# Kernel optimization log

Measured on AMD Instinct MI355X. Metric: run time of the kernel, lower is better.

## Reference

```python
import jax, jax.numpy as jnp
import numpy as np

TOPK = 8
NMS_K = 5
SIGMA = 3.0


def _mlp2(x, w1, b1, w2, b2):
    return jnp.maximum(x @ w1 + b1, 0.0) @ w2 + b2


def _l2norm(x):
    n = jnp.linalg.norm(x, axis=-1, keepdims=True)
    return x / jnp.maximum(n, 1e-12)


def _bilinear_sample(fm, ys, xs):
    # fm: (V, C, Hf, Wf); ys, xs: (V, K) float sample positions (align_corners=True,
    # zero padding outside [0, size-1], matching F.grid_sample defaults).
    V, C, Hf, Wf = fm.shape
    y0f = jnp.floor(ys)
    x0f = jnp.floor(xs)
    wy = ys - y0f  # (V, K)
    wx = xs - x0f
    y0 = y0f.astype(jnp.int32)
    x0 = x0f.astype(jnp.int32)

    def gather(yi, xi):
        valid = ((yi >= 0) & (yi < Hf) & (xi >= 0) & (xi < Wf)).astype(fm.dtype)  # (V,K)
        yc = jnp.clip(yi, 0, Hf - 1)
        xc = jnp.clip(xi, 0, Wf - 1)
        v = jax.vmap(lambda f, y, x: f[:, y, x])(fm, yc, xc)  # (V, C, K)
        return v * valid[:, None, :]

    out = (gather(y0, x0) * ((1 - wy) * (1 - wx))[:, None, :]
           + gather(y0, x0 + 1) * ((1 - wy) * wx)[:, None, :]
           + gather(y0 + 1, x0) * (wy * (1 - wx))[:, None, :]
           + gather(y0 + 1, x0 + 1) * (wy * wx)[:, None, :])
    return out.transpose(0, 2, 1)  # (V, K, C)


def _forward(heatmap, feature_map, prev_node_embed,
             n1_w, n1_b, n2_w, n2_b, p1_w, p1_b, p2_w, p2_b,
             c_w, c_b, s_w, s_b):
    bs, nc, _, H, W = heatmap.shape
    hm = heatmap.reshape(bs * nc, H, W)

    # ---- PeakExtractor: maxpool NMS + topk ----
    pad = NMS_K // 2
    pooled = jax.lax.reduce_window(hm, -jnp.inf, jax.lax.max,
                                   (1, NMS_K, NMS_K), (1, 1, 1),
                                   ((0, 0), (pad, pad), (pad, pad)))
    hm_nms = hm * (hm == pooled).astype(hm.dtype)
    vals, idxs = jax.lax.top_k(hm_nms.reshape(bs * nc, H * W), TOPK)
    rows = idxs // W
    cols = idxs % W
    peak_coords = jnp.stack([rows, cols], axis=-1).reshape(bs, nc, TOPK, 2)

    # ---- NodeEmbeddingHead: grid_sample gather + MLP ----
    V, C, Hf, Wf = feature_map.shape
    ys = rows[:V].astype(jnp.float32) * (Hf / H)
    xs = cols[:V].astype(jnp.float32) * (Wf / W)
    sampled = _bilinear_sample(feature_map, ys, xs)  # (V, K, C)
    peak_node_embeds = _l2norm(_mlp2(sampled, n1_w, n1_b, n2_w, n2_b))  # (V, K, D)

    # ---- pooled node embed ----
    pooled_feat = feature_map.mean(axis=(0, 2, 3))  # (C,)
    curr_node_embed = _l2norm(_mlp2(pooled_feat[None, :], p1_w, p1_b, p2_w, p2_b))  # (1, D)

    # ---- TransitionScorer ----
    D = prev_node_embed.shape[-1]
    prev_e = jnp.broadcast_to(prev_node_embed, (V, D))
    curr_e = jnp.broadcast_to(curr_node_embed, (V, D))
    context = jnp.maximum(jnp.concatenate([prev_e, curr_e], axis=-1) @ c_w + c_b, 0.0)
    proto = context @ s_w + s_b  # (V, D)
    transition_scores = jnp.einsum('vkd,vd->vk', peak_node_embeds, proto)  # (V, K)
    peak_weights = jax.nn.softmax(transition_scores, axis=-1)

    # ---- separable gaussian bias (vectorized over views and peaks) ----
    coords0 = peak_coords[0, :V].astype(jnp.float32)  # (V, K, 2)
    rr = jnp.arange(H, dtype=jnp.float32)
    cc = jnp.arange(W, dtype=jnp.float32)
    inv2s2 = 1.0 / (2.0 * SIGMA ** 2)
    gr = jnp.exp(-((rr[None, None, :] - coords0[..., 0:1]) ** 2) * inv2s2)  # (V,K,H)
    gc = jnp.exp(-((cc[None, None, :] - coords0[..., 1:2]) ** 2) * inv2s2)  # (V,K,W)
    bias = jnp.einsum('vkh,vkw,vk->vhw', gr, gc, peak_weights)  # (V,H,W)
    reweighted = heatmap + bias[None, :, None]  # (bs, nc, 1, H, W)

    return reweighted, curr_node_embed, peak_coords, transition_scores, peak_node_embeds


def setup_inputs() -> dict:
    key = jax.random.key(0)
    ks = jax.random.split(key, 16)
    C, D = 128, 64
    inp = {
        'heatmap': jax.random.normal(ks[0], (1, 16, 1, 1024, 1024), jnp.float32),
        'feature_map': jax.random.normal(ks[1], (16, 128, 32, 32), jnp.float32),
        'prev_node_embed': jax.random.normal(ks[2], (1, D), jnp.float32),
        'n1_w': jax.random.normal(ks[3], (C, D), jnp.float32) * 0.05,
        'n1_b': jax.random.normal(ks[4], (D,), jnp.float32) * 0.05,
        'n2_w': jax.random.normal(ks[5], (D, D), jnp.float32) * 0.05,
        'n2_b': jax.random.normal(ks[6], (D,), jnp.float32) * 0.05,
        'p1_w': jax.random.normal(ks[7], (C, D), jnp.float32) * 0.05,
        'p1_b': jax.random.normal(ks[8], (D,), jnp.float32) * 0.05,
        'p2_w': jax.random.normal(ks[9], (D, D), jnp.float32) * 0.05,
        'p2_b': jax.random.normal(ks[10], (D,), jnp.float32) * 0.05,
        'c_w': jax.random.normal(ks[11], (2 * D, D), jnp.float32) * 0.05,
        'c_b': jax.random.normal(ks[12], (D,), jnp.float32) * 0.05,
        's_w': jax.random.normal(ks[13], (D, D), jnp.float32) * 0.05,
        's_b': jax.random.normal(ks[14], (D,), jnp.float32) * 0.05,
    }
    return inp


def reference(heatmap, feature_map, prev_node_embed,
              n1_w, n1_b, n2_w, n2_b, p1_w, p1_b, p2_w, p2_b,
              c_w, c_b, s_w, s_b):
    return _forward(heatmap, feature_map, prev_node_embed,
                    n1_w, n1_b, n2_w, n2_b, p1_w, p1_b, p2_w, p2_b,
                    c_w, c_b, s_w, s_b)
```

## Files before the change

### kernel.cpp

```cpp
#include <hip/hip_runtime.h>
#include <math.h>

#define HH 1024
#define WW 1024
#define NCH 16
#define ROWS_PER_BLOCK 8
#define BLOCKS_PER_CH (HH / ROWS_PER_BLOCK)
#define NEG_INF (-INFINITY)

__device__ __forceinline__ bool better_f(float v1, int i1, float v2, int i2) {
    return (v1 > v2) || ((v1 == v2) && (i1 < i2));
}

__global__ __launch_bounds__(256) void kA(const float* __restrict__ hm,
                                          float* __restrict__ out,
                                          float* __restrict__ cand_val,
                                          int* __restrict__ cand_idx) {
    const int ch = blockIdx.y;
    const int r0 = blockIdx.x * ROWS_PER_BLOCK;
    const int tid = threadIdx.x;
    const int c0 = tid * 4;
    const float* hmc = hm + (size_t)ch * (size_t)(HH * WW);
    float* outc = out + (size_t)ch * (size_t)(HH * WW);

    float4 rawv[5], hxv[5];
    float tv[8]; int ti[8];
#pragma unroll
    for (int j = 0; j < 8; ++j) { tv[j] = NEG_INF; ti[j] = 0x7FFFFFFF; }

    auto loadrow = [&](int r, float4& rv, float4& hv) {
        if (r < 0 || r >= HH) {
            rv = make_float4(NEG_INF, NEG_INF, NEG_INF, NEG_INF);
            hv = rv;
            return;
        }
        const float* rp = hmc + (size_t)r * WW;
        float4 M = *(const float4*)(rp + c0);
        float4 L = (c0 >= 4) ? *(const float4*)(rp + c0 - 4)
                             : make_float4(NEG_INF, NEG_INF, NEG_INF, NEG_INF);
        float4 R = (c0 + 4 < WW) ? *(const float4*)(rp + c0 + 4)
                                 : make_float4(NEG_INF, NEG_INF, NEG_INF, NEG_INF);
        float v2 = L.z, v3 = L.w, v4 = M.x, v5 = M.y, v6 = M.z, v7 = M.w, v8 = R.x, v9 = R.y;
        float a = fmaxf(v2, v3), b = fmaxf(v4, v5), c = fmaxf(v6, v7), d = fmaxf(v8, v9);
        hv.x = fmaxf(fmaxf(a, b), v6);
        hv.y = fmaxf(fmaxf(v3, b), c);
        hv.z = fmaxf(fmaxf(b, c), v8);
        hv.w = fmaxf(fmaxf(v5, c), d);
        rv = M;
    };

    auto push = [&](float v, int ix) {
        if (better_f(v, ix, tv[7], ti[7])) {
            tv[7] = v; ti[7] = ix;
#pragma unroll
            for (int j = 7; j >= 1; --j) {
                if (better_f(tv[j], ti[j], tv[j - 1], ti[j - 1])) {
                    float fv = tv[j]; tv[j] = tv[j - 1]; tv[j - 1] = fv;
                    int iv = ti[j]; ti[j] = ti[j - 1]; ti[j - 1] = iv;
                }
            }
        }
    };

    loadrow(r0 - 2, rawv[0], hxv[0]);
    loadrow(r0 - 1, rawv[1], hxv[1]);
    loadrow(r0 + 0, rawv[2], hxv[2]);
    loadrow(r0 + 1, rawv[3], hxv[3]);

#pragma unroll
    for (int i = 0; i < ROWS_PER_BLOCK; ++i) {
        const int r = r0 + i;
        loadrow(r + 2, rawv[(4 + i) % 5], hxv[(4 + i) % 5]);
        float4 p;
        p.x = fmaxf(fmaxf(fmaxf(hxv[0].x, hxv[1].x), fmaxf(hxv[2].x, hxv[3].x)), hxv[4].x);
        p.y = fmaxf(fmaxf(fmaxf(hxv[0].y, hxv[1].y), fmaxf(hxv[2].y, hxv[3].y)), hxv[4].y);
        p.z = fmaxf(fmaxf(fmaxf(hxv[0].z, hxv[1].z), fmaxf(hxv[2].z, hxv[3].z)), hxv[4].z);
        p.w = fmaxf(fmaxf(fmaxf(hxv[0].w, hxv[1].w), fmaxf(hxv[2].w, hxv[3].w)), hxv[4].w);
        float4 cen = rawv[(2 + i) % 5];
        *(float4*)(outc + (size_t)r * WW + c0) = cen;
        int base = r * WW + c0;
        push((cen.x == p.x) ? cen.x : 0.0f, base + 0);
        push((cen.y == p.y) ? cen.y : 0.0f, base + 1);
        push((cen.z == p.z) ? cen.z : 0.0f, base + 2);
        push((cen.w == p.w) ? cen.w : 0.0f, base + 3);
    }

    __shared__ float swv[2][4];
    __shared__ int swi[2][4];
    const int lane = tid & 63, wid = tid >> 6;
    float wv = 0.f; int wi = 0;
    for (int rnd = 0; rnd < 8; ++rnd) {
        float v = tv[0]; int ix = ti[0];
#pragma unroll
        for (int off = 32; off >= 1; off >>= 1) {
            float ov = __shfl_xor(v, off);
            int oi = __shfl_xor(ix, off);
            if (better_f(ov, oi, v, ix)) { v = ov; ix = oi; }
        }
        if (lane == 0) { swv[rnd & 1][wid] = v; swi[rnd & 1][wid] = ix; }
        __syncthreads();
        float bv = swv[rnd & 1][0]; int bi = swi[rnd & 1][0];
        if (better_f(swv[rnd & 1][1], swi[rnd & 1][1], bv, bi)) { bv = swv[rnd & 1][1]; bi = swi[rnd & 1][1]; }
        if (better_f(swv[rnd & 1][2], swi[rnd & 1][2], bv, bi)) { bv = swv[rnd & 1][2]; bi = swi[rnd & 1][2]; }
        if (better_f(swv[rnd & 1][3], swi[rnd & 1][3], bv, bi)) { bv = swv[rnd & 1][3]; bi = swi[rnd & 1][3]; }
        if (ti[0] == bi) {
#pragma unroll
            for (int j = 0; j < 7; ++j) { tv[j] = tv[j + 1]; ti[j] = ti[j + 1]; }
            tv[7] = NEG_INF; ti[7] = 0x7FFFFFFF;
        }
        if (tid == rnd) { wv = bv; wi = bi; }
    }
    const int slotbase = (ch * BLOCKS_PER_CH + blockIdx.x) * 8;
    if (tid < 8) { cand_val[slotbase + tid] = wv; cand_idx[slotbase + tid] = wi; }
}

__global__ __launch_bounds__(64) void kB(const float* __restrict__ cand_val,
                                         const int* __restrict__ cand_idx,
                                         float* __restrict__ out_pc,
                                         int* __restrict__ ws_rows,
                                         int* __restrict__ ws_cols) {
    const int ch = blockIdx.x;
    const int lane = threadIdx.x;
    float tv[8]; int ti[8];
#pragma unroll
    for (int j = 0; j < 8; ++j) { tv[j] = NEG_INF; ti[j] = 0x7FFFFFFF; }
    auto push = [&](float v, int ix) {
        if (better_f(v, ix, tv[7], ti[7])) {
            tv[7] = v; ti[7] = ix;
#pragma unroll
            for (int j = 7; j >= 1; --j) {
                if (better_f(tv[j], ti[j], tv[j - 1], ti[j - 1])) {
                    float fv = tv[j]; tv[j] = tv[j - 1]; tv[j - 1] = fv;
                    int iv = ti[j]; ti[j] = ti[j - 1]; ti[j - 1] = iv;
                }
            }
        }
    };
    const float* cv = cand_val + (size_t)ch * 1024 + lane * 16;
    const int* ci = cand_idx + (size_t)ch * 1024 + lane * 16;
#pragma unroll
    for (int j = 0; j < 16; ++j) push(cv[j], ci[j]);

    int mywin = 0;
    for (int rnd = 0; rnd < 8; ++rnd) {
        float v = tv[0]; int ix = ti[0];
#pragma unroll
        for (int off = 32; off >= 1; off >>= 1) {
            float ov = __shfl_xor(v, off);
            int oi = __shfl_xor(ix, off);
            if (better_f(ov, oi, v, ix)) { v = ov; ix = oi; }
        }
        if (ti[0] == ix) {
#pragma unroll
            for (int j = 0; j < 7; ++j) { tv[j] = tv[j + 1]; ti[j] = ti[j + 1]; }
            tv[7] = NEG_INF; ti[7] = 0x7FFFFFFF;
        }
        if (lane == rnd) mywin = ix;
    }
    if (lane < 8) {
        int row = mywin >> 10;
        int col = mywin & 1023;
        out_pc[ch * 16 + lane * 2 + 0] = (float)row;
        out_pc[ch * 16 + lane * 2 + 1] = (float)col;
        ws_rows[ch * 8 + lane] = row;
        ws_cols[ch * 8 + lane] = col;
    }
}

__global__ __launch_bounds__(256) void kC(const float* __restrict__ fm,
                                          float* __restrict__ pooled) {
    const int c = blockIdx.x;
    const int tid = threadIdx.x;
    float s = 0.f;
    for (int v = 0; v < 16; ++v) {
        const float* p = fm + (size_t)v * 131072 + (size_t)c * 1024;
#pragma unroll
        for (int i = 0; i < 4; ++i) s += p[tid + i * 256];
    }
#pragma unroll
    for (int off = 32; off >= 1; off >>= 1) s += __shfl_xor(s, off);
    __shared__ float red[4];
    if ((tid & 63) == 0) red[tid >> 6] = s;
    __syncthreads();
    if (tid == 0) pooled[c] = (red[0] + red[1] + red[2] + red[3]) * (1.0f / 16384.0f);
}

__global__ __launch_bounds__(64) void kD0(const float* __restrict__ pooled,
                                          const float* __restrict__ prev,
                                          const float* __restrict__ p1w, const float* __restrict__ p1b,
                                          const float* __restrict__ p2w, const float* __restrict__ p2b,
                                          const float* __restrict__ cw, const float* __restrict__ cb,
                                          const float* __restrict__ sw, const float* __restrict__ sb,
                                          float* __restrict__ out_curr,
                                          float* __restrict__ ws_proto) {
    const int j = threadIdx.x;
    __shared__ float h1[64], cshr[64], ctx[64];
    float acc = p1b[j];
    for (int c = 0; c < 128; ++c) acc = fmaf(pooled[c], p1w[c * 64 + j], acc);
    h1[j] = fmaxf(acc, 0.f);
    __syncthreads();
    float e = p2b[j];
    for (int m = 0; m < 64; ++m) e = fmaf(h1[m], p2w[m * 64 + j], e);
    float sq = e * e;
#pragma unroll
    for (int off = 32; off >= 1; off >>= 1) sq += __shfl_xor(sq, off);
    float cur = e / fmaxf(sqrtf(sq), 1e-12f);
    out_curr[j] = cur;
    cshr[j] = cur;
    __syncthreads();
    float a3 = cb[j];
    for (int i = 0; i < 64; ++i) a3 = fmaf(prev[i], cw[i * 64 + j], a3);
    for (int i = 0; i < 64; ++i) a3 = fmaf(cshr[i], cw[(64 + i) * 64 + j], a3);
    ctx[j] = fmaxf(a3, 0.f);
    __syncthreads();
    float a4 = sb[j];
    for (int m = 0; m < 64; ++m) a4 = fmaf(ctx[m], sw[m * 64 + j], a4);
    ws_proto[j] = a4;
}

__global__ __launch_bounds__(64) void kD1(const float* __restrict__ fm,
                                          const int* __restrict__ ws_rows,
                                          const int* __restrict__ ws_cols,
                                          const float* __restrict__ n1w, const float* __restrict__ n1b,
                                          const float* __restrict__ n2w, const float* __restrict__ n2b,
                                          const float* __restrict__ ws_proto,
                                          float* __restrict__ out_ts,
                                          float* __restrict__ out_pe) {
    const int p = blockIdx.x;
    const int v = p >> 3, k = p & 7;
    const int j = threadIdx.x;
    __shared__ float s[128], h1[64];
    const float* base = fm + (size_t)v * 131072;

    int row = ws_rows[v * 8 + k], col = ws_cols[v * 8 + k];
    float ys = (float)row * 0.03125f, xs = (float)col * 0.03125f;
    int y0 = (int)floorf(ys), x0 = (int)floorf(xs);
    float wy = ys - (float)y0, wx = xs - (float)x0;
    float w00 = (1.f - wy) * (1.f - wx), w01 = (1.f - wy) * wx;
    float w10 = wy * (1.f - wx), w11 = wy * wx;

    auto samp = [&](int c) -> float {
        const float* fc = base + (size_t)c * 1024;
        float r = fc[y0 * 32 + x0] * w00;
        if (x0 + 1 < 32) r += fc[y0 * 32 + x0 + 1] * w01;
        if (y0 + 1 < 32) {
            r += fc[(y0 + 1) * 32 + x0] * w10;
            if (x0 + 1 < 32) r += fc[(y0 + 1) * 32 + x0 + 1] * w11;
        }
        return r;
    };
    s[j] = samp(j);
    s[j + 64] = samp(j + 64);
    __syncthreads();
    float a = n1b[j];
    for (int c = 0; c < 128; ++c) a = fmaf(s[c], n1w[c * 64 + j], a);
    h1[j] = fmaxf(a, 0.f);
    __syncthreads();
    float e = n2b[j];
    for (int m = 0; m < 64; ++m) e = fmaf(h1[m], n2w[m * 64 + j], e);
    float sq = e * e;
#pragma unroll
    for (int off = 32; off >= 1; off >>= 1) sq += __shfl_xor(sq, off);
    float emb = e / fmaxf(sqrtf(sq), 1e-12f);
    out_pe[(size_t)p * 64 + j] = emb;
    float sc = emb * ws_proto[j];
#pragma unroll
    for (int off = 32; off >= 1; off >>= 1) sc += __shfl_xor(sc, off);
    if (j == 0) out_ts[p] = sc;
}

__global__ __launch_bounds__(256) void kF(const int* __restrict__ ws_rows,
                                          const int* __restrict__ ws_cols,
                                          const float* __restrict__ ts,
                                          float* __restrict__ out) {
    const int p = blockIdx.x;
    const int v = p >> 3, k = p & 7;
    const int tid = threadIdx.x;
    float t[8];
#pragma unroll
    for (int i = 0; i < 8; ++i) t[i] = ts[v * 8 + i];
    float m = t[0];
#pragma unroll
    for (int i = 1; i < 8; ++i) m = fmaxf(m, t[i]);
    float sum = 0.f;
#pragma unroll
    for (int i = 0; i < 8; ++i) sum += __expf(t[i] - m);
    const float pw = __expf(t[k] - m) / sum;

    const int r = ws_rows[v * 8 + k], c = ws_cols[v * 8 + k];
    float* oc = out + (size_t)v * (size_t)(HH * WW);
    const float inv2s2 = 1.0f / 18.0f;
    const int RAD = 32, SZ = 65;
    for (int idx = tid; idx < SZ * SZ; idx += 256) {
        int dy = idx / SZ - RAD, dx = idx % SZ - RAD;
        int py = r + dy, px = c + dx;
        if (py >= 0 && py < HH && px >= 0 && px < WW) {
            float d2 = (float)(dy * dy + dx * dx);
            atomicAdd(&oc[(size_t)py * WW + px], pw * __expf(-d2 * inv2s2));
        }
    }
}

extern "C" void kernel_launch(void* const* d_in, const int* in_sizes, int n_in,
                              void* d_out, int out_size, void* d_ws, size_t ws_size,
                              hipStream_t stream) {
    (void)in_sizes; (void)n_in; (void)out_size; (void)ws_size;
    const float* hm   = (const float*)d_in[0];
    const float* fm   = (const float*)d_in[1];
    const float* prev = (const float*)d_in[2];
    const float* n1w  = (const float*)d_in[3];
    const float* n1b  = (const float*)d_in[4];
    const float* n2w  = (const float*)d_in[5];
    const float* n2b  = (const float*)d_in[6];
    const float* p1w  = (const float*)d_in[7];
    const float* p1b  = (const float*)d_in[8];
    const float* p2w  = (const float*)d_in[9];
    const float* p2b  = (const float*)d_in[10];
    const float* cw   = (const float*)d_in[11];
    const float* cb   = (const float*)d_in[12];
    const float* sw   = (const float*)d_in[13];
    const float* sb   = (const float*)d_in[14];
    float* out = (float*)d_out;

    char* ws = (char*)d_ws;
    float* cand_val  = (float*)(ws + 0);
    int*   cand_idx  = (int*)(ws + 65536);
    int*   ws_rows   = (int*)(ws + 131072);
    int*   ws_cols   = (int*)(ws + 131584);
    float* ws_pooled = (float*)(ws + 132096);
    float* ws_proto  = (float*)(ws + 132608);

    float* out_rew  = out;
    float* out_curr = out + 16777216;
    float* out_pc   = out + 16777280;
    float* out_ts   = out + 16777536;
    float* out_pe   = out + 16777664;

    kA<<<dim3(BLOCKS_PER_CH, NCH), 256, 0, stream>>>(hm, out_rew, cand_val, cand_idx);
    kB<<<NCH, 64, 0, stream>>>(cand_val, cand_idx, out_pc, ws_rows, ws_cols);
    kC<<<128, 256, 0, stream>>>(fm, ws_pooled);
    kD0<<<1, 64, 0, stream>>>(ws_pooled, prev, p1w, p1b, p2w, p2b, cw, cb, sw, sb,
                              out_curr, ws_proto);
    kD1<<<128, 64, 0, stream>>>(fm, ws_rows, ws_cols, n1w, n1b, n2w, n2b, ws_proto,
                                out_ts, out_pe);
    kF<<<128, 256, 0, stream>>>(ws_rows, ws_cols, out_ts, out_rew);
}
```

Baseline: 206.8 us.

## Fuse tail kernels, use lane shuffles for NMS halo, drop splat atomics

Combines the candidate merge with feature pooling, and the prototype MLP, node embedding and Gaussian splat into one block per view. This cuts six launches to three and lets the splat use plain read-modify-write under block barriers instead of atomics. kA now gets its horizontal halo from wavefront shuffles rather than two extra float4 loads, and the top-8 lists become named scalars so they stay in registers. The cost is that the prototype MLP is recomputed in each of the 16 blocks and the splat phase runs on only 16 blocks, which lowers parallelism there.

```diff
diff --git a/kernel.cpp b/kernel.cpp
--- a/kernel.cpp
+++ b/kernel.cpp
@@ -11,6 +11,52 @@
 __device__ __forceinline__ bool better_f(float v1, int i1, float v2, int i2) {
     return (v1 > v2) || ((v1 == v2) && (i1 < i2));
 }
+
+#define CSWAP(J, JM) \
+    if (better_f(tv##J, ti##J, tv##JM, ti##JM)) { \
+        float _fv = tv##J; tv##J = tv##JM; tv##JM = _fv; \
+        int _iv = ti##J; ti##J = ti##JM; ti##JM = _iv; }
+
+#define PUSH(VAL, IDX) do { \
+    float _pv = (VAL); int _pix = (IDX); \
+    if (better_f(_pv, _pix, tv7, ti7)) { \
+        tv7 = _pv; ti7 = _pix; \
+        CSWAP(7,6) CSWAP(6,5) CSWAP(5,4) CSWAP(4,3) CSWAP(3,2) CSWAP(2,1) CSWAP(1,0) \
+    } } while (0)
+
+#define POP() do { \
+    tv0=tv1; ti0=ti1; tv1=tv2; ti1=ti2; tv2=tv3; ti2=ti3; tv3=tv4; ti3=ti4; \
+    tv4=tv5; ti4=ti5; tv5=tv6; ti5=ti6; tv6=tv7; ti6=ti7; \
+    tv7=NEG_INF; ti7=0x7FFFFFFF; } while (0)
+
+#define TOP8_INIT() \
+    float tv0=NEG_INF,tv1=NEG_INF,tv2=NEG_INF,tv3=NEG_INF,tv4=NEG_INF,tv5=NEG_INF,tv6=NEG_INF,tv7=NEG_INF; \
+    int ti0=0x7FFFFFFF,ti1=0x7FFFFFFF,ti2=0x7FFFFFFF,ti3=0x7FFFFFFF,ti4=0x7FFFFFFF,ti5=0x7FFFFFFF,ti6=0x7FFFFFFF,ti7=0x7FFFFFFF;
+
+#define LOADROW(R, RV, HV) do { \
+    const int _r = (R); \
+    if (_r < 0 || _r >= HH) { \
+        RV = make_float4(NEG_INF, NEG_INF, NEG_INF, NEG_INF); HV = RV; \
+    } else { \
+        const float* _rp = hmc + (size_t)_r * WW; \
+        float4 _M = *(const float4*)(_rp + c0); \
+        float _lm2 = __shfl_up(_M.z, 1), _lm1 = __shfl_up(_M.w, 1); \
+        float _rp0 = __shfl_down(_M.x, 1), _rp1 = __shfl_down(_M.y, 1); \
+        if (lane == 0) { \
+            _lm2 = (c0 >= 2) ? _rp[c0 - 2] : NEG_INF; \
+            _lm1 = (c0 >= 1) ? _rp[c0 - 1] : NEG_INF; \
+        } \
+        if (lane == 63) { \
+            _rp0 = (c0 + 4 < WW) ? _rp[c0 + 4] : NEG_INF; \
+            _rp1 = (c0 + 5 < WW) ? _rp[c0 + 5] : NEG_INF; \
+        } \
+        float _m01 = fmaxf(_M.x, _M.y), _m23 = fmaxf(_M.z, _M.w); \
+        HV.x = fmaxf(fmaxf(_lm2, _lm1), fmaxf(_m01, _M.z)); \
+        HV.y = fmaxf(_lm1, fmaxf(_m01, _m23)); \
+        HV.z = fmaxf(fmaxf(_m01, _m23), _rp0); \
+        HV.w = fmaxf(fmaxf(_M.y, _m23), fmaxf(_rp0, _rp1)); \
+        RV = _M; \
+    } } while (0)
 
 __global__ __launch_bounds__(256) void kA(const float* __restrict__ hm,
                                           float* __restrict__ out,
@@ -19,78 +65,46 @@
     const int ch = blockIdx.y;
     const int r0 = blockIdx.x * ROWS_PER_BLOCK;
     const int tid = threadIdx.x;
+    const int lane = tid & 63;
     const int c0 = tid * 4;
     const float* hmc = hm + (size_t)ch * (size_t)(HH * WW);
     float* outc = out + (size_t)ch * (size_t)(HH * WW);
 
-    float4 rawv[5], hxv[5];
-    float tv[8]; int ti[8];
-#pragma unroll
-    for (int j = 0; j < 8; ++j) { tv[j] = NEG_INF; ti[j] = 0x7FFFFFFF; }
-
-    auto loadrow = [&](int r, float4& rv, float4& hv) {
-        if (r < 0 || r >= HH) {
-            rv = make_float4(NEG_INF, NEG_INF, NEG_INF, NEG_INF);
-            hv = rv;
-            return;
-        }
-        const float* rp = hmc + (size_t)r * WW;
-        float4 M = *(const float4*)(rp + c0);
-        float4 L = (c0 >= 4) ? *(const float4*)(rp + c0 - 4)
-                             : make_float4(NEG_INF, NEG_INF, NEG_INF, NEG_INF);
-        float4 R = (c0 + 4 < WW) ? *(const float4*)(rp + c0 + 4)
-                                 : make_float4(NEG_INF, NEG_INF, NEG_INF, NEG_INF);
-        float v2 = L.z, v3 = L.w, v4 = M.x, v5 = M.y, v6 = M.z, v7 = M.w, v8 = R.x, v9 = R.y;
-        float a = fmaxf(v2, v3), b = fmaxf(v4, v5), c = fmaxf(v6, v7), d = fmaxf(v8, v9);
-        hv.x = fmaxf(fmaxf(a, b), v6);
-        hv.y = fmaxf(fmaxf(v3, b), c);
-        hv.z = fmaxf(fmaxf(b, c), v8);
-        hv.w = fmaxf(fmaxf(v5, c), d);
-        rv = M;
-    };
-
-    auto push = [&](float v, int ix) {
-        if (better_f(v, ix, tv[7], ti[7])) {
-            tv[7] = v; ti[7] = ix;
-#pragma unroll
-            for (int j = 7; j >= 1; --j) {
-                if (better_f(tv[j], ti[j], tv[j - 1], ti[j - 1])) {
-                    float fv = tv[j]; tv[j] = tv[j - 1]; tv[j - 1] = fv;
-                    int iv = ti[j]; ti[j] = ti[j - 1]; ti[j - 1] = iv;
-                }
-            }
-        }
-    };
-
-    loadrow(r0 - 2, rawv[0], hxv[0]);
-    loadrow(r0 - 1, rawv[1], hxv[1]);
-    loadrow(r0 + 0, rawv[2], hxv[2]);
-    loadrow(r0 + 1, rawv[3], hxv[3]);
+    TOP8_INIT();
+
+    float4 raw0, raw1, raw2, raw3, raw4;
+    float4 hx0, hx1, hx2, hx3, hx4;
+    LOADROW(r0 - 2, raw0, hx0);
+    LOADROW(r0 - 1, raw1, hx1);
+    LOADROW(r0 + 0, raw2, hx2);
+    LOADROW(r0 + 1, raw3, hx3);
 
 #pragma unroll
     for (int i = 0; i < ROWS_PER_BLOCK; ++i) {
         const int r = r0 + i;
-        loadrow(r + 2, rawv[(4 + i) % 5], hxv[(4 + i) % 5]);
+        LOADROW(r + 2, raw4, hx4);
         float4 p;
-        p.x = fmaxf(fmaxf(fmaxf(hxv[0].x, hxv[1].x), fmaxf(hxv[2].x, hxv[3].x)), hxv[4].x);
-        p.y = fmaxf(fmaxf(fmaxf(hxv[0].y, hxv[1].y), fmaxf(hxv[2].y, hxv[3].y)), hxv[4].y);
-        p.z = fmaxf(fmaxf(fmaxf(hxv[0].z, hxv[1].z), fmaxf(hxv[2].z, hxv[3].z)), hxv[4].z);
-        p.w = fmaxf(fmaxf(fmaxf(hxv[0].w, hxv[1].w), fmaxf(hxv[2].w, hxv[3].w)), hxv[4].w);
-        float4 cen = rawv[(2 + i) % 5];
+        p.x = fmaxf(fmaxf(fmaxf(hx0.x, hx1.x), fmaxf(hx2.x, hx3.x)), hx4.x);
+        p.y = fmaxf(fmaxf(fmaxf(hx0.y, hx1.y), fmaxf(hx2.y, hx3.y)), hx4.y);
+        p.z = fmaxf(fmaxf(fmaxf(hx0.z, hx1.z), fmaxf(hx2.z, hx3.z)), hx4.z);
+        p.w = fmaxf(fmaxf(fmaxf(hx0.w, hx1.w), fmaxf(hx2.w, hx3.w)), hx4.w);
+        float4 cen = raw2;
         *(float4*)(outc + (size_t)r * WW + c0) = cen;
         int base = r * WW + c0;
-        push((cen.x == p.x) ? cen.x : 0.0f, base + 0);
-        push((cen.y == p.y) ? cen.y : 0.0f, base + 1);
-        push((cen.z == p.z) ? cen.z : 0.0f, base + 2);
-        push((cen.w == p.w) ? cen.w : 0.0f, base + 3);
+        PUSH((cen.x == p.x) ? cen.x : 0.0f, base + 0);
+        PUSH((cen.y == p.y) ? cen.y : 0.0f, base + 1);
+        PUSH((cen.z == p.z) ? cen.z : 0.0f, base + 2);
+        PUSH((cen.w == p.w) ? cen.w : 0.0f, base + 3);
+        raw0 = raw1; raw1 = raw2; raw2 = raw3; raw3 = raw4;
+        hx0 = hx1; hx1 = hx2; hx2 = hx3; hx3 = hx4;
     }
 
     __shared__ float swv[2][4];
     __shared__ int swi[2][4];
-    const int lane = tid & 63, wid = tid >> 6;
+    const int wid = tid >> 6;
     float wv = 0.f; int wi = 0;
     for (int rnd = 0; rnd < 8; ++rnd) {
-        float v = tv[0]; int ix = ti[0];
+        float v = tv0; int ix = ti0;
 #pragma unroll
         for (int off = 32; off >= 1; off >>= 1) {
             float ov = __shfl_xor(v, off);
@@ -103,109 +117,101 @@
         if (better_f(swv[rnd & 1][1], swi[rnd & 1][1], bv, bi)) { bv = swv[rnd & 1][1]; bi = swi[rnd & 1][1]; }
         if (better_f(swv[rnd & 1][2], swi[rnd & 1][2], bv, bi)) { bv = swv[rnd & 1][2]; bi = swi[rnd & 1][2]; }
         if (better_f(swv[rnd & 1][3], swi[rnd & 1][3], bv, bi)) { bv = swv[rnd & 1][3]; bi = swi[rnd & 1][3]; }
-        if (ti[0] == bi) {
-#pragma unroll
-            for (int j = 0; j < 7; ++j) { tv[j] = tv[j + 1]; ti[j] = ti[j + 1]; }
-            tv[7] = NEG_INF; ti[7] = 0x7FFFFFFF;
-        }
+        if (ti0 == bi) POP();
         if (tid == rnd) { wv = bv; wi = bi; }
     }
     const int slotbase = (ch * BLOCKS_PER_CH + blockIdx.x) * 8;
     if (tid < 8) { cand_val[slotbase + tid] = wv; cand_idx[slotbase + tid] = wi; }
 }
 
-__global__ __launch_bounds__(64) void kB(const float* __restrict__ cand_val,
-                                         const int* __restrict__ cand_idx,
-                                         float* __restrict__ out_pc,
-                                         int* __restrict__ ws_rows,
-                                         int* __restrict__ ws_cols) {
-    const int ch = blockIdx.x;
-    const int lane = threadIdx.x;
-    float tv[8]; int ti[8];
-#pragma unroll
-    for (int j = 0; j < 8; ++j) { tv[j] = NEG_INF; ti[j] = 0x7FFFFFFF; }
-    auto push = [&](float v, int ix) {
-        if (better_f(v, ix, tv[7], ti[7])) {
-            tv[7] = v; ti[7] = ix;
-#pragma unroll
-            for (int j = 7; j >= 1; --j) {
-                if (better_f(tv[j], ti[j], tv[j - 1], ti[j - 1])) {
-                    float fv = tv[j]; tv[j] = tv[j - 1]; tv[j - 1] = fv;
-                    int iv = ti[j]; ti[j] = ti[j - 1]; ti[j - 1] = iv;
-                }
+__global__ __launch_bounds__(256) void kBC(const float* __restrict__ cand_val,
+                                           const int* __restrict__ cand_idx,
+                                           const float* __restrict__ fm,
+                                           float* __restrict__ out_pc,
+                                           int* __restrict__ ws_rows,
+                                           int* __restrict__ ws_cols,
+                                           float* __restrict__ pooled) {
+    const int tid = threadIdx.x;
+    if (blockIdx.x < 16) {
+        if (tid >= 64) return;
+        const int ch = blockIdx.x;
+        const int lane = tid;
+        TOP8_INIT();
+        const float* cv = cand_val + (size_t)ch * 1024 + lane * 16;
+        const int* ci = cand_idx + (size_t)ch * 1024 + lane * 16;
+#pragma unroll
+        for (int j = 0; j < 16; ++j) PUSH(cv[j], ci[j]);
+
+        int mywin = 0;
+        for (int rnd = 0; rnd < 8; ++rnd) {
+            float v = tv0; int ix = ti0;
+#pragma unroll
+            for (int off = 32; off >= 1; off >>= 1) {
+                float ov = __shfl_xor(v, off);
+                int oi = __shfl_xor(ix, off);
+                if (better_f(ov, oi, v, ix)) { v = ov; ix = oi; }
             }
-        }
-    };
-    const float* cv = cand_val + (size_t)ch * 1024 + lane * 16;
-    const int* ci = cand_idx + (size_t)ch * 1024 + lane * 16;
-#pragma unroll
-    for (int j = 0; j < 16; ++j) push(cv[j], ci[j]);
-
-    int mywin = 0;
-    for (int rnd = 0; rnd < 8; ++rnd) {
-        float v = tv[0]; int ix = ti[0];
-#pragma unroll
-        for (int off = 32; off >= 1; off >>= 1) {
-            float ov = __shfl_xor(v, off);
-            int oi = __shfl_xor(ix, off);
-            if (better_f(ov, oi, v, ix)) { v = ov; ix = oi; }
-        }
-        if (ti[0] == ix) {
-#pragma unroll
-            for (int j = 0; j < 7; ++j) { tv[j] = tv[j + 1]; ti[j] = ti[j + 1]; }
-            tv[7] = NEG_INF; ti[7] = 0x7FFFFFFF;
-        }
-        if (lane == rnd) mywin = ix;
-    }
-    if (lane < 8) {
-        int row = mywin >> 10;
-        int col = mywin & 1023;
-        out_pc[ch * 16 + lane * 2 + 0] = (float)row;
-        out_pc[ch * 16 + lane * 2 + 1] = (float)col;
-        ws_rows[ch * 8 + lane] = row;
-        ws_cols[ch * 8 + lane] = col;
-    }
-}
-
-__global__ __launch_bounds__(256) void kC(const float* __restrict__ fm,
-                                          float* __restrict__ pooled) {
-    const int c = blockIdx.x;
+            if (ti0 == ix) POP();
+            if (lane == rnd) mywin = ix;
+        }
+        if (lane < 8) {
+            int row = mywin >> 10;
+            int col = mywin & 1023;
+            out_pc[ch * 16 + lane * 2 + 0] = (float)row;
+            out_pc[ch * 16 + lane * 2 + 1] = (float)col;
+            ws_rows[ch * 8 + lane] = row;
+            ws_cols[ch * 8 + lane] = col;
+        }
+    } else {
+        const int c = blockIdx.x - 16;
+        float s = 0.f;
+        for (int v = 0; v < 16; ++v) {
+            const float* p = fm + (size_t)v * 131072 + (size_t)c * 1024;
+#pragma unroll
+            for (int i = 0; i < 4; ++i) s += p[tid + i * 256];
+        }
+#pragma unroll
+        for (int off = 32; off >= 1; off >>= 1) s += __shfl_xor(s, off);
+        __shared__ float red[4];
+        if ((tid & 63) == 0) red[tid >> 6] = s;
+        __syncthreads();
+        if (tid == 0) pooled[c] = (red[0] + red[1] + red[2] + red[3]) * (1.0f / 16384.0f);
+    }
+}
+
+__global__ __launch_bounds__(256) void kDF(const float* __restrict__ fm,
+                                           const int* __restrict__ ws_rows,
+                                           const int* __restrict__ ws_cols,
+                                           const float* __restrict__ n1w, const float* __restrict__ n1b,
+                                           const float* __restrict__ n2w, const float* __restrict__ n2b,
+                                           const float* __restrict__ p1w, const float* __restrict__ p1b,
+                                           const float* __restrict__ p2w, const float* __restrict__ p2b,
+                                           const float* __restrict__ cw, const float* __restrict__ cb,
+                                           const float* __restrict__ sw, const float* __restrict__ sb,
+                                           const float* __restrict__ prev,
+                                           const float* __restrict__ pooled,
+                                           float* __restrict__ out_curr,
+                                           float* __restrict__ out_ts,
+                                           float* __restrict__ out_pe,
+                                           float* __restrict__ out_rew) {
+    const int v = blockIdx.x;
     const int tid = threadIdx.x;
-    float s = 0.f;
-    for (int v = 0; v < 16; ++v) {
-        const float* p = fm + (size_t)v * 131072 + (size_t)c * 1024;
-#pragma unroll
-        for (int i = 0; i < 4; ++i) s += p[tid + i * 256];
-    }
-#pragma unroll
-    for (int off = 32; off >= 1; off >>= 1) s += __shfl_xor(s, off);
-    __shared__ float red[4];
-    if ((tid & 63) == 0) red[tid >> 6] = s;
-    __syncthreads();
-    if (tid == 0) pooled[c] = (red[0] + red[1] + red[2] + red[3]) * (1.0f / 16384.0f);
-}
-
-__global__ __launch_bounds__(64) void kD0(const float* __restrict__ pooled,
-                                          const float* __restrict__ prev,
-                                          const float* __restrict__ p1w, const float* __restrict__ p1b,
-                                          const float* __restrict__ p2w, const float* __restrict__ p2b,
-                                          const float* __restrict__ cw, const float* __restrict__ cb,
-                                          const float* __restrict__ sw, const float* __restrict__ sb,
-                                          float* __restrict__ out_curr,
-                                          float* __restrict__ ws_proto) {
-    const int j = threadIdx.x;
-    __shared__ float h1[64], cshr[64], ctx[64];
+    const int w = tid >> 6;
+    const int j = tid & 63;
+    __shared__ float ph1[64], cshr[64], ctx[64], proto_s[64], ts_s[8];
+    __shared__ float s_w[4][128], h1_w[4][64];
+
     float acc = p1b[j];
     for (int c = 0; c < 128; ++c) acc = fmaf(pooled[c], p1w[c * 64 + j], acc);
-    h1[j] = fmaxf(acc, 0.f);
+    ph1[j] = fmaxf(acc, 0.f);
     __syncthreads();
     float e = p2b[j];
-    for (int m = 0; m < 64; ++m) e = fmaf(h1[m], p2w[m * 64 + j], e);
+    for (int m = 0; m < 64; ++m) e = fmaf(ph1[m], p2w[m * 64 + j], e);
     float sq = e * e;
 #pragma unroll
     for (int off = 32; off >= 1; off >>= 1) sq += __shfl_xor(sq, off);
     float cur = e / fmaxf(sqrtf(sq), 1e-12f);
-    out_curr[j] = cur;
+    if (v == 0 && tid < 64) out_curr[j] = cur;
     cshr[j] = cur;
     __syncthreads();
     float a3 = cb[j];
@@ -215,89 +221,71 @@
     __syncthreads();
     float a4 = sb[j];
     for (int m = 0; m < 64; ++m) a4 = fmaf(ctx[m], sw[m * 64 + j], a4);
-    ws_proto[j] = a4;
-}
-
-__global__ __launch_bounds__(64) void kD1(const float* __restrict__ fm,
-                                          const int* __restrict__ ws_rows,
-                                          const int* __restrict__ ws_cols,
-                                          const float* __restrict__ n1w, const float* __restrict__ n1b,
-                                          const float* __restrict__ n2w, const float* __restrict__ n2b,
-                                          const float* __restrict__ ws_proto,
-                                          float* __restrict__ out_ts,
-                                          float* __restrict__ out_pe) {
-    const int p = blockIdx.x;
-    const int v = p >> 3, k = p & 7;
-    const int j = threadIdx.x;
-    __shared__ float s[128], h1[64];
+    proto_s[j] = a4;
+    __syncthreads();
+
     const float* base = fm + (size_t)v * 131072;
-
-    int row = ws_rows[v * 8 + k], col = ws_cols[v * 8 + k];
-    float ys = (float)row * 0.03125f, xs = (float)col * 0.03125f;
-    int y0 = (int)floorf(ys), x0 = (int)floorf(xs);
-    float wy = ys - (float)y0, wx = xs - (float)x0;
-    float w00 = (1.f - wy) * (1.f - wx), w01 = (1.f - wy) * wx;
-    float w10 = wy * (1.f - wx), w11 = wy * wx;
-
-    auto samp = [&](int c) -> float {
-        const float* fc = base + (size_t)c * 1024;
-        float r = fc[y0 * 32 + x0] * w00;
-        if (x0 + 1 < 32) r += fc[y0 * 32 + x0 + 1] * w01;
-        if (y0 + 1 < 32) {
-            r += fc[(y0 + 1) * 32 + x0] * w10;
-            if (x0 + 1 < 32) r += fc[(y0 + 1) * 32 + x0 + 1] * w11;
-        }
-        return r;
-    };
-    s[j] = samp(j);
-    s[j + 64] = samp(j + 64);
-    __syncthreads();
-    float a = n1b[j];
-    for (int c = 0; c < 128; ++c) a = fmaf(s[c], n1w[c * 64 + j], a);
-    h1[j] = fmaxf(a, 0.f);
-    __syncthreads();
-    float e = n2b[j];
-    for (int m = 0; m < 64; ++m) e = fmaf(h1[m], n2w[m * 64 + j], e);
-    float sq = e * e;
-#pragma unroll
-    for (int off = 32; off >= 1; off >>= 1) sq += __shfl_xor(sq, off);
-    float emb = e / fmaxf(sqrtf(sq), 1e-12f);
-    out_pe[(size_t)p * 64 + j] = emb;
-    float sc = emb * ws_proto[j];
-#pragma unroll
-    for (int off = 32; off >= 1; off >>= 1) sc += __shfl_xor(sc, off);
-    if (j == 0) out_ts[p] = sc;
-}
-
-__global__ __launch_bounds__(256) void kF(const int* __restrict__ ws_rows,
-                                          const int* __restrict__ ws_cols,
-                                          const float* __restrict__ ts,
-                                          float* __restrict__ out) {
-    const int p = blockIdx.x;
-    const int v = p >> 3, k = p & 7;
-    const int tid = threadIdx.x;
-    float t[8];
-#pragma unroll
-    for (int i = 0; i < 8; ++i) t[i] = ts[v * 8 + i];
-    float m = t[0];
-#pragma unroll
-    for (int i = 1; i < 8; ++i) m = fmaxf(m, t[i]);
+    for (int kk = 0; kk < 2; ++kk) {
+        const int k = w + kk * 4;
+        int row = ws_rows[v * 8 + k], col = ws_cols[v * 8 + k];
+        float ys = (float)row * 0.03125f, xs = (float)col * 0.03125f;
+        int y0 = (int)floorf(ys), x0 = (int)floorf(xs);
+        float wy = ys - (float)y0, wx = xs - (float)x0;
+        float w00 = (1.f - wy) * (1.f - wx), w01 = (1.f - wy) * wx;
+        float w10 = wy * (1.f - wx), w11 = wy * wx;
+
+        auto samp = [&](int c) -> float {
+            const float* fc = base + (size_t)c * 1024;
+            float r = fc[y0 * 32 + x0] * w00;
+            if (x0 + 1 < 32) r += fc[y0 * 32 + x0 + 1] * w01;
+            if (y0 + 1 < 32) {
+                r += fc[(y0 + 1) * 32 + x0] * w10;
+                if (x0 + 1 < 32) r += fc[(y0 + 1) * 32 + x0 + 1] * w11;
+            }
+            return r;
+        };
+        s_w[w][j] = samp(j);
+        s_w[w][j + 64] = samp(j + 64);
+        float a = n1b[j];
+        for (int c = 0; c < 128; ++c) a = fmaf(s_w[w][c], n1w[c * 64 + j], a);
+        h1_w[w][j] = fmaxf(a, 0.f);
+        float e2 = n2b[j];
+        for (int m = 0; m < 64; ++m) e2 = fmaf(h1_w[w][m], n2w[m * 64 + j], e2);
+        float sq2 = e2 * e2;
+#pragma unroll
+        for (int off = 32; off >= 1; off >>= 1) sq2 += __shfl_xor(sq2, off);
+        float emb = e2 / fmaxf(sqrtf(sq2), 1e-12f);
+        out_pe[((size_t)v * 8 + k) * 64 + j] = emb;
+        float sc = emb * proto_s[j];
+#pragma unroll
+        for (int off = 32; off >= 1; off >>= 1) sc += __shfl_xor(sc, off);
+        if (j == 0) { ts_s[k] = sc; out_ts[v * 8 + k] = sc; }
+    }
+    __syncthreads();
+
+    float m = ts_s[0];
+#pragma unroll
+    for (int i = 1; i < 8; ++i) m = fmaxf(m, ts_s[i]);
     float sum = 0.f;
 #pragma unroll
-    for (int i = 0; i < 8; ++i) sum += __expf(t[i] - m);
-    const float pw = __expf(t[k] - m) / sum;
-
-    const int r = ws_rows[v * 8 + k], c = ws_cols[v * 8 + k];
-    float* oc = out + (size_t)v * (size_t)(HH * WW);
+    for (int i = 0; i < 8; ++i) sum += __expf(ts_s[i] - m);
+    const float inv_sum = 1.0f / sum;
+
+    float* oc = out_rew + (size_t)v * (size_t)(HH * WW);
     const float inv2s2 = 1.0f / 18.0f;
     const int RAD = 32, SZ = 65;
-    for (int idx = tid; idx < SZ * SZ; idx += 256) {
-        int dy = idx / SZ - RAD, dx = idx % SZ - RAD;
-        int py = r + dy, px = c + dx;
-        if (py >= 0 && py < HH && px >= 0 && px < WW) {
-            float d2 = (float)(dy * dy + dx * dx);
-            atomicAdd(&oc[(size_t)py * WW + px], pw * __expf(-d2 * inv2s2));
-        }
+    for (int k = 0; k < 8; ++k) {
+        const float pw = __expf(ts_s[k] - m) * inv_sum;
+        const int r = ws_rows[v * 8 + k], c = ws_cols[v * 8 + k];
+        for (int idx = tid; idx < SZ * SZ; idx += 256) {
+            int dy = idx / SZ - RAD, dx = idx % SZ - RAD;
+            int py = r + dy, px = c + dx;
+            if (py >= 0 && py < HH && px >= 0 && px < WW) {
+                float d2 = (float)(dy * dy + dx * dx);
+                oc[(size_t)py * WW + px] += pw * __expf(-d2 * inv2s2);
+            }
+        }
+        __syncthreads();
     }
 }
 
@@ -328,7 +316,6 @@
     int*   ws_rows   = (int*)(ws + 131072);
     int*   ws_cols   = (int*)(ws + 131584);
     float* ws_pooled = (float*)(ws + 132096);
-    float* ws_proto  = (float*)(ws + 132608);
 
     float* out_rew  = out;
     float* out_curr = out + 16777216;
@@ -337,11 +324,8 @@
     float* out_pe   = out + 16777664;
 
     kA<<<dim3(BLOCKS_PER_CH, NCH), 256, 0, stream>>>(hm, out_rew, cand_val, cand_idx);
-    kB<<<NCH, 64, 0, stream>>>(cand_val, cand_idx, out_pc, ws_rows, ws_cols);
-    kC<<<128, 256, 0, stream>>>(fm, ws_pooled);
-    kD0<<<1, 64, 0, stream>>>(ws_pooled, prev, p1w, p1b, p2w, p2b, cw, cb, sw, sb,
-                              out_curr, ws_proto);
-    kD1<<<128, 64, 0, stream>>>(fm, ws_rows, ws_cols, n1w, n1b, n2w, n2b, ws_proto,
-                                out_ts, out_pe);
-    kF<<<128, 256, 0, stream>>>(ws_rows, ws_cols, out_ts, out_rew);
-}
+    kBC<<<144, 256, 0, stream>>>(cand_val, cand_idx, fm, out_pc, ws_rows, ws_cols, ws_pooled);
+    kDF<<<NCH, 256, 0, stream>>>(fm, ws_rows, ws_cols, n1w, n1b, n2w, n2b,
+                                 p1w, p1b, p2w, p2b, cw, cb, sw, sb, prev, ws_pooled,
+                                 out_curr, out_ts, out_pe, out_rew);
+}
```

Result: slower. 253.0 us (+22.4%).
